# Kernel optimization log

Hardware: AMD Instinct MI355X
Metric: run time of the kernel (lower is better)

Reference implementation:

```python
import jax, jax.numpy as jnp
import numpy as np

B, N, D = 4, 2048, 1024
H, DH = 16, 64
MAX_POS_EMB = 256
TOPK = 64


def setup_inputs() -> dict:
    key = jax.random.key(0)
    ks = jax.random.split(key, 8)
    s = 0.02
    inner = H * DH
    return {
        "x": jax.random.normal(ks[0], (B, N, D), jnp.float32),
        "gating_mask": jax.random.uniform(ks[1], (B, 1, N, 1), jnp.float32),
        "Wq": jax.random.normal(ks[2], (D, inner), jnp.float32) * s,
        "bq": jnp.zeros((inner,), jnp.float32),
        "Wkv": jax.random.normal(ks[3], (D, 2 * inner), jnp.float32) * s,
        "bkv": jnp.zeros((2 * inner,), jnp.float32),
        "Wo": jax.random.normal(ks[4], (inner, D), jnp.float32) * s,
        "bo": jnp.zeros((D,), jnp.float32),
        "rel_emb": jax.random.normal(ks[5], (MAX_POS_EMB, DH), jnp.float32) * s,
        "mask": jnp.ones((B, N), bool),
        "sparse_topk": TOPK,
    }


def reference(x, gating_mask, Wq, bq, Wkv, bkv, Wo, bo, rel_emb, mask, sparse_topk):
    b, n, d = x.shape
    h, dh = H, DH
    scale = dh ** -0.5
    mask_val = -jnp.finfo(x.dtype).max

    # projections -> [b, h, n, dh]
    q = (x @ Wq + bq).reshape(b, n, h, dh).transpose(0, 2, 1, 3)
    kv = x @ Wkv + bkv
    k = kv[..., : h * dh].reshape(b, n, h, dh).transpose(0, 2, 1, 3)
    v = kv[..., h * dh:].reshape(b, n, h, dh).transpose(0, 2, 1, 3)

    dots = jnp.einsum("bhid,bhjd->bhij", q, k) * scale  # [b,h,n,n]

    # relative positional bias: q . E[clip(i-j+M, 0, M-1)]
    seq = jnp.arange(n)
    dist = jnp.clip(seq[:, None] - seq[None, :] + MAX_POS_EMB, 0, MAX_POS_EMB - 1)
    qE = jnp.einsum("bhid,rd->bhir", q, rel_emb) * scale  # [b,h,n,R]
    pos_attn = jnp.take_along_axis(qE, dist[None, None, :, :], axis=-1)  # [b,h,n,n]
    dots = dots + pos_attn

    # padding mask: mask_i * mask_j
    full_mask = mask[:, None, :, None] & mask[:, None, None, :]
    dots = jnp.where(full_mask, dots, mask_val)

    # topk sparsification: keep only scores >= k-th largest per row
    top = jax.lax.top_k(dots, sparse_topk)[0]  # [b,h,n,topk]
    vk = top[..., -1:]
    dots = jnp.where(dots < vk, mask_val, dots)

    attn = jax.nn.softmax(dots, axis=-1)
    attn = attn * gating_mask

    out = jnp.einsum("bhij,bhjd->bhid", attn, v)
    out = out.transpose(0, 2, 1, 3).reshape(b, n, h * dh)
    return out @ Wo + bo
```

## Files before the change

### kernel.cpp

```cpp
#include <hip/hip_runtime.h>
#include <stdint.h>


typedef __attribute__((ext_vector_type(8))) short short8;
typedef __attribute__((ext_vector_type(4))) float floatx4;

#define Bn   4
#define Nn   2048
#define Hn   16
#define BHn  (Bn*Hn)
#define DELTA 0.00125f

__device__ __forceinline__ float bf2f(unsigned short u) {
  union { unsigned int i; float f; } v; v.i = ((unsigned int)u) << 16; return v.f;
}
__device__ __forceinline__ unsigned short f2bf(float f) {
  union { float f; unsigned int i; } v; v.f = f;
  unsigned int r = v.i + 0x7fffu + ((v.i >> 16) & 1u);
  return (unsigned short)(r >> 16);
}
__device__ __forceinline__ floatx4 mfma16(short8 a, short8 b, floatx4 c) {
  return __builtin_amdgcn_mfma_f32_16x16x32_bf16(a, b, c, 0, 0, 0);
}
__device__ __forceinline__ void split2(float x, unsigned short& h, unsigned short& m) {
  h = f2bf(x);
  m = f2bf(x - bf2f(h));
}
__device__ __forceinline__ void split3(float x, unsigned short& h, unsigned short& m, unsigned short& l) {
  h = f2bf(x);
  float r = x - bf2f(h);
  m = f2bf(r);
  l = f2bf(r - bf2f(m));
}

__global__ __launch_bounds__(256)
void transpose_split3(const float* __restrict__ W,
                      unsigned short* __restrict__ T0,
                      unsigned short* __restrict__ T1,
                      unsigned short* __restrict__ T2,
                      int K, int Ncols)
{
  __shared__ float tile[32][33];
  int k0 = blockIdx.y * 32, n0 = blockIdx.x * 32;
  int tx = threadIdx.x & 31, ty = threadIdx.x >> 5;
  for (int s = 0; s < 32; s += 8)
    tile[ty + s][tx] = W[(size_t)(k0 + ty + s) * Ncols + n0 + tx];
  __syncthreads();
  for (int s = 0; s < 32; s += 8) {
    float x = tile[tx][ty + s];
    unsigned short h, m, l;
    split3(x, h, m, l);
    size_t o = (size_t)(n0 + ty + s) * K + k0 + tx;
    T0[o] = h; T1[o] = m; T2[o] = l;
  }
}

__global__ __launch_bounds__(256)
void transpose_split2(const float* __restrict__ W,
                      unsigned short* __restrict__ T0,
                      unsigned short* __restrict__ T1,
                      int K, int Ncols)
{
  __shared__ float tile[32][33];
  int k0 = blockIdx.y * 32, n0 = blockIdx.x * 32;
  int tx = threadIdx.x & 31, ty = threadIdx.x >> 5;
  for (int s = 0; s < 32; s += 8)
    tile[ty + s][tx] = W[(size_t)(k0 + ty + s) * Ncols + n0 + tx];
  __syncthreads();
  for (int s = 0; s < 32; s += 8) {
    float x = tile[tx][ty + s];
    unsigned short h, m;
    split2(x, h, m);
    size_t o = (size_t)(n0 + ty + s) * K + k0 + tx;
    T0[o] = h; T1[o] = m;
  }
}

__global__ __launch_bounds__(256)
void convert_bf16(const float* __restrict__ in, unsigned short* __restrict__ outp, int n) {
  int i = blockIdx.x * 256 + threadIdx.x;
  if (i < n) outp[i] = f2bf(in[i]);
}

__global__ __launch_bounds__(256)
void gemm_qkv(const float* __restrict__ A,
              const unsigned short* __restrict__ B0,
              const unsigned short* __restrict__ B1,
              const unsigned short* __restrict__ B2,
              const float* __restrict__ bias,
              float* __restrict__ O32,
              unsigned short* __restrict__ Oh,
              unsigned short* __restrict__ Om,
              unsigned short* __restrict__ Vh,
              int K, float scale)
{
  __shared__ unsigned short lA[3][128 * 40];
  __shared__ unsigned short lB[3][128 * 40];
  const int tid = threadIdx.x;
  const int lane = tid & 63;
  const int m0 = blockIdx.y * 128, n0 = blockIdx.x * 128;
  const int wid = tid >> 6, wm = wid >> 1, wn = wid & 1;
  const int fr = lane & 15, fq = lane >> 4;
  floatx4 acc[4][4] = {};

  for (int k0 = 0; k0 < K; k0 += 32) {
    __syncthreads();
    #pragma unroll
    for (int p = 0; p < 2; p++) {
      int c = tid + p * 256;
      int row = c >> 2, kc = (c & 3) * 8;
      size_t go = (size_t)(m0 + row) * K + k0 + kc;
      float4 v0 = *(const float4*)&A[go];
      float4 v1 = *(const float4*)&A[go + 4];
      union { unsigned short u[8]; uint4 q; } hh, mm, ll;
      float xs[8] = {v0.x, v0.y, v0.z, v0.w, v1.x, v1.y, v1.z, v1.w};
      #pragma unroll
      for (int e = 0; e < 8; e++) split3(xs[e], hh.u[e], mm.u[e], ll.u[e]);
      *(uint4*)&lA[0][row * 40 + kc] = hh.q;
      *(uint4*)&lA[1][row * 40 + kc] = mm.q;
      *(uint4*)&lA[2][row * 40 + kc] = ll.q;
      size_t bo = (size_t)(n0 + row) * K + k0 + kc;
      *(uint4*)&lB[0][row * 40 + kc] = *(const uint4*)&B0[bo];
      *(uint4*)&lB[1][row * 40 + kc] = *(const uint4*)&B1[bo];
      *(uint4*)&lB[2][row * 40 + kc] = *(const uint4*)&B2[bo];
    }
    __syncthreads();
    short8 af[3][4], bfr[3][4];
    #pragma unroll
    for (int s = 0; s < 3; s++)
      #pragma unroll
      for (int t = 0; t < 4; t++) {
        af[s][t]  = *(const short8*)&lA[s][(wm * 64 + t * 16 + fr) * 40 + 8 * fq];
        bfr[s][t] = *(const short8*)&lB[s][(wn * 64 + t * 16 + fr) * 40 + 8 * fq];
      }
    #pragma unroll
    for (int mi = 0; mi < 4; mi++)
      #pragma unroll
      for (int ni = 0; ni < 4; ni++) {
        acc[mi][ni] = mfma16(af[0][mi], bfr[0][ni], acc[mi][ni]);
        acc[mi][ni] = mfma16(af[0][mi], bfr[1][ni], acc[mi][ni]);
        acc[mi][ni] = mfma16(af[1][mi], bfr[0][ni], acc[mi][ni]);
        acc[mi][ni] = mfma16(af[1][mi], bfr[1][ni], acc[mi][ni]);
        acc[mi][ni] = mfma16(af[0][mi], bfr[2][ni], acc[mi][ni]);
        acc[mi][ni] = mfma16(af[2][mi], bfr[0][ni], acc[mi][ni]);
      }
  }
  #pragma unroll
  for (int mi = 0; mi < 4; mi++)
    #pragma unroll
    for (int ni = 0; ni < 4; ni++) {
      int nl = n0 + wn * 64 + ni * 16 + fr;
      float bv = bias[nl];
      #pragma unroll
      for (int rg = 0; rg < 4; rg++) {
        int ml = m0 + wm * 64 + mi * 16 + fq * 4 + rg;
        float val = (acc[mi][ni][rg] + bv) * scale;
        int bb = ml >> 11, ii = ml & 2047;
        int hh2 = (nl & 1023) >> 6, dd = nl & 63;
        size_t idx = (((size_t)bb * Hn + hh2) * Nn + ii) * 64 + dd;
        if (nl < 1024) {
          O32[idx] = val;
          unsigned short h, m;
          split2(val, h, m);
          Oh[idx] = h; Om[idx] = m;
        } else {
          Vh[idx] = f2bf(val);
        }
      }
    }
}

__global__ __launch_bounds__(256)
void gemm_out(const float* __restrict__ A,
              const unsigned short* __restrict__ B0,
              const unsigned short* __restrict__ B1,
              const float* __restrict__ bias,
              float* __restrict__ O32,
              int Ncols, int K)
{
  __shared__ unsigned short lA[2][128 * 40];
  __shared__ unsigned short lB[2][128 * 40];
  const int tid = threadIdx.x;
  const int lane = tid & 63;
  const int m0 = blockIdx.y * 128, n0 = blockIdx.x * 128;
  const int wid = tid >> 6, wm = wid >> 1, wn = wid & 1;
  const int fr = lane & 15, fq = lane >> 4;
  floatx4 acc[4][4] = {};

  for (int k0 = 0; k0 < K; k0 += 32) {
    __syncthreads();
    #pragma unroll
    for (int p = 0; p < 2; p++) {
      int c = tid + p * 256;
      int row = c >> 2, kc = (c & 3) * 8;
      size_t go = (size_t)(m0 + row) * K + k0 + kc;
      float4 v0 = *(const float4*)&A[go];
      float4 v1 = *(const float4*)&A[go + 4];
      union { unsigned short u[8]; uint4 q; } hh, mm;
      float xs[8] = {v0.x, v0.y, v0.z, v0.w, v1.x, v1.y, v1.z, v1.w};
      #pragma unroll
      for (int e = 0; e < 8; e++) split2(xs[e], hh.u[e], mm.u[e]);
      *(uint4*)&lA[0][row * 40 + kc] = hh.q;
      *(uint4*)&lA[1][row * 40 + kc] = mm.q;
      size_t bo = (size_t)(n0 + row) * K + k0 + kc;
      *(uint4*)&lB[0][row * 40 + kc] = *(const uint4*)&B0[bo];
      *(uint4*)&lB[1][row * 40 + kc] = *(const uint4*)&B1[bo];
    }
    __syncthreads();
    short8 af[2][4], bfr[2][4];
    #pragma unroll
    for (int s = 0; s < 2; s++)
      #pragma unroll
      for (int t = 0; t < 4; t++) {
        af[s][t]  = *(const short8*)&lA[s][(wm * 64 + t * 16 + fr) * 40 + 8 * fq];
        bfr[s][t] = *(const short8*)&lB[s][(wn * 64 + t * 16 + fr) * 40 + 8 * fq];
      }
    #pragma unroll
    for (int mi = 0; mi < 4; mi++)
      #pragma unroll
      for (int ni = 0; ni < 4; ni++) {
        acc[mi][ni] = mfma16(af[0][mi], bfr[0][ni], acc[mi][ni]);
        acc[mi][ni] = mfma16(af[0][mi], bfr[1][ni], acc[mi][ni]);
        acc[mi][ni] = mfma16(af[1][mi], bfr[0][ni], acc[mi][ni]);
      }
  }
  #pragma unroll
  for (int mi = 0; mi < 4; mi++)
    #pragma unroll
    for (int ni = 0; ni < 4; ni++) {
      int nl = n0 + wn * 64 + ni * 16 + fr;
      float bv = bias[nl];
      #pragma unroll
      for (int rg = 0; rg < 4; rg++) {
        int ml = m0 + wm * 64 + mi * 16 + fq * 4 + rg;
        O32[(size_t)ml * Ncols + nl] = acc[mi][ni][rg] + bv;
      }
    }
}

__global__ __launch_bounds__(512, 4)
void attn_k(const unsigned short* __restrict__ qh,
            const unsigned short* __restrict__ qm,
            const unsigned short* __restrict__ kh,
            const unsigned short* __restrict__ km,
            const unsigned short* __restrict__ vh,
            const float* __restrict__ q32,
            const float* __restrict__ k32,
            const unsigned short* __restrict__ relbf,
            const float* __restrict__ rel32,
            const float* __restrict__ gating,
            const int* __restrict__ topkp,
            float* __restrict__ inner)
{
  extern __shared__ char smem[];
  _Float16* S = (_Float16*)smem;
  unsigned short* KtH = (unsigned short*)(smem + 65536);
  unsigned short* KtM = KtH + 4096;
  _Float16* qE = (_Float16*)KtH;

  const int ib = blockIdx.x, bh = blockIdx.y;
  const int i0 = ib * 16;
  const int b = bh >> 4, h = bh & 15;
  const int tid = threadIdx.x;
  const int lane = tid & 63, w = tid >> 6;
  const int fr = lane & 15, fq = lane >> 4;
  const int topk = topkp[0];

  const size_t qoff = ((size_t)bh * Nn + i0) * 64;
  const size_t qf = qoff + (size_t)fr * 64 + 8 * fq;
  const short8 aqh0 = *(const short8*)&qh[qf];
  const short8 aqh1 = *(const short8*)&qh[qf + 32];
  const short8 aqm0 = *(const short8*)&qm[qf];
  const short8 aqm1 = *(const short8*)&qm[qf + 32];

  for (int jt = 0; jt < 32; jt++) {
    __syncthreads();
    {
      int row = tid >> 3, dc = (tid & 7) * 8;
      size_t g = ((size_t)bh * Nn + jt * 64 + row) * 64 + dc;
      *(uint4*)&KtH[row * 64 + dc] = *(const uint4*)&kh[g];
      *(uint4*)&KtM[row * 64 + dc] = *(const uint4*)&km[g];
    }
    __syncthreads();
    if ((jt & 1) == (w >> 2)) {
      int wc = w & 3;
      int kb = (wc * 16 + fr) * 64 + 8 * fq;
      short8 kh0 = *(const short8*)&KtH[kb];
      short8 kh1 = *(const short8*)&KtH[kb + 32];
      short8 km0 = *(const short8*)&KtM[kb];
      short8 km1 = *(const short8*)&KtM[kb + 32];
      floatx4 c = {};
      c = mfma16(aqh0, kh0, c); c = mfma16(aqh1, kh1, c);
      c = mfma16(aqh0, km0, c); c = mfma16(aqh1, km1, c);
      c = mfma16(aqm0, kh0, c); c = mfma16(aqm1, kh1, c);
      #pragma unroll
      for (int rg = 0; rg < 4; rg++)
        S[(fq * 4 + rg) * 2048 + jt * 64 + wc * 16 + fr] = (_Float16)c[rg];
    }
  }
  __syncthreads();

  #pragma unroll
  for (int rs = 0; rs < 2; rs++) {
    int r0 = (w * 2 + rs) * 16;
    size_t rf = (size_t)(r0 + fr) * 64 + 8 * fq;
    short8 rb0 = *(const short8*)&relbf[rf];
    short8 rb1 = *(const short8*)&relbf[rf + 32];
    floatx4 c = {};
    c = mfma16(aqh0, rb0, c); c = mfma16(aqh1, rb1, c);
    c = mfma16(aqm0, rb0, c); c = mfma16(aqm1, rb1, c);
    #pragma unroll
    for (int rg = 0; rg < 4; rg++)
      qE[(fq * 4 + rg) * 256 + r0 + fr] = (_Float16)c[rg];
  }
  __syncthreads();

  #pragma unroll 1
  for (int rr = 0; rr < 2; rr++) {
    const int r = w * 2 + rr;
    const int i = i0 + r;
    const _Float16* Srow = S + r * 2048;
    const _Float16* qErow = qE + r * 256;

    float key[32];
    float mx = -3.0e38f, sum = 0.f, ssq = 0.f;
    #pragma unroll
    for (int e = 0; e < 16; e++) {
      int j0 = 2 * lane + 128 * e;
      union { unsigned int u; _Float16 hx[2]; } sv;
      sv.u = *(const unsigned int*)&Srow[j0];
      int r0i = i - j0 + 256;
      int c0 = r0i < 0 ? 0 : (r0i > 255 ? 255 : r0i);
      int r1i = r0i - 1;
      int c1 = r1i < 0 ? 0 : (r1i > 255 ? 255 : r1i);
      float s0 = (float)sv.hx[0] + (float)qErow[c0];
      float s1 = (float)sv.hx[1] + (float)qErow[c1];
      key[2 * e] = s0; key[2 * e + 1] = s1;
      mx = fmaxf(mx, fmaxf(s0, s1));
      sum += s0 + s1;
      ssq += s0 * s0 + s1 * s1;
    }
    #pragma unroll
    for (int d = 1; d < 64; d <<= 1) {
      mx = fmaxf(mx, __shfl_xor(mx, d));
      sum += __shfl_xor(sum, d);
      ssq += __shfl_xor(ssq, d);
    }
    const float mu = sum * (1.f / 2048.f);
    const float sg = sqrtf(fmaxf(ssq * (1.f / 2048.f) - mu * mu, 0.f)) + 1e-9f;

    auto cntGE = [&](float u) -> int {
      int c = 0;
      #pragma unroll
      for (int e = 0; e < 32; e++) c += (key[e] >= u) ? 1 : 0;
      #pragma unroll
      for (int d = 1; d < 64; d <<= 1) c += __shfl_xor(c, d);
      return c;
    };

    float lo = mu + 1.6f * sg;
    float hi = mx + fabsf(mx) * 1e-6f + 1e-20f;
    int cl = cntGE(lo);
    #pragma unroll 1
    for (int t = 0; t < 6 && cl < topk; t++) {
      hi = lo; lo -= (0.8f + 0.4f * t) * sg; cl = cntGE(lo);
    }
    if (cl < topk) lo = -3.0e38f;
    #pragma unroll 1
    for (int it = 0; it < 10; it++) {
      float mid = 0.5f * (lo + hi);
      if (cntGE(mid) >= topk) lo = mid; else hi = mid;
    }
    const float C = hi + 2.0f * DELTA;
    const float L = lo - 2.0f * DELTA;

    char* sb = (char*)Srow;
    float* Pl = (float*)(sb);
    int*   Jl = (int*)(sb + 512);
    float* Sx = (float*)(sb + 1024);
    int*   Jc = (int*)(sb + 1280);
    asm volatile("" ::: "memory");
    const unsigned long long lmlt = (1ull << lane) - 1ull;

    int base = 0;
    #pragma unroll
    for (int e2 = 0; e2 < 32; e2++) {
      bool dk = key[e2] >= C;
      unsigned long long mk = __ballot(dk);
      if (dk) {
        int pos = base + __popcll(mk & lmlt);
        Pl[pos] = key[e2]; Jl[pos] = 2 * lane + 128 * (e2 >> 1) + (e2 & 1);
      }
      base += __popcll(mk);
    }
    int mcand = 0;
    #pragma unroll
    for (int e2 = 0; e2 < 32; e2++) {
      bool cd = (key[e2] >= L) && (key[e2] < C);
      unsigned long long mk = __ballot(cd);
      if (cd) {
        int pos = mcand + __popcll(mk & lmlt);
        if (pos < 64) Jc[pos] = 2 * lane + 128 * (e2 >> 1) + (e2 & 1);
      }
      mcand += __popcll(mk);
    }
    if (mcand > 64) mcand = 64;
    asm volatile("" ::: "memory");

    const size_t qrow = ((size_t)bh * Nn + i) * 64 + lane;
    const double qv = (double)q32[qrow];
    #pragma unroll 1
    for (int c2 = 0; c2 < mcand; c2++) {
      int j = Jc[c2];
      int ridx = i - j + 256;
      ridx = ridx < 0 ? 0 : (ridx > 255 ? 255 : ridx);
      size_t krow = ((size_t)bh * Nn + j) * 64 + lane;
      double t = qv * ((double)k32[krow] + (double)rel32[ridx * 64 + lane]);
      #pragma unroll
      for (int d = 1; d < 64; d <<= 1) t += __shfl_xor(t, d);
      if (lane == 0) Sx[c2] = (float)t;
    }
    asm volatile("" ::: "memory");

    const int need = topk - base;
    float myx = (lane < mcand) ? Sx[lane] : -3.0e38f;
    int rank = 0;
    #pragma unroll 1
    for (int c2 = 0; c2 < mcand; c2++) {
      float o = Sx[c2];
      rank += (o > myx || (o == myx && c2 < lane)) ? 1 : 0;
    }
    bool ck = (lane < mcand) && (rank < need);
    unsigned long long mk2 = __ballot(ck);
    if (ck) {
      int pos = base + __popcll(mk2 & lmlt);
      Pl[pos] = myx; Jl[pos] = Jc[lane];
    }
    base += __popcll(mk2);
    const int nk = base;
    asm volatile("" ::: "memory");

    float p = 0.f;
    if (lane < nk) { p = __expf(Pl[lane] - mx); Pl[lane] = p; }
    float psum = p;
    #pragma unroll
    for (int d = 1; d < 64; d <<= 1) psum += __shfl_xor(psum, d);
    const float coef = gating[(size_t)b * Nn + i] / psum;
    asm volatile("" ::: "memory");

    float a0 = 0, a1 = 0, a2 = 0, a3 = 0;
    const size_t vb = (size_t)bh * Nn * 64;
    int t4 = nk & ~3;
    #pragma unroll 1
    for (int t = 0; t < t4; t += 4) {
      float p0 = Pl[t], p1 = Pl[t + 1], p2 = Pl[t + 2], p3 = Pl[t + 3];
      int j0 = Jl[t], j1 = Jl[t + 1], j2 = Jl[t + 2], j3 = Jl[t + 3];
      a0 += p0 * bf2f(vh[vb + (size_t)j0 * 64 + lane]);
      a1 += p1 * bf2f(vh[vb + (size_t)j1 * 64 + lane]);
      a2 += p2 * bf2f(vh[vb + (size_t)j2 * 64 + lane]);
      a3 += p3 * bf2f(vh[vb + (size_t)j3 * 64 + lane]);
    }
    for (int t = t4; t < nk; t++)
      a0 += Pl[t] * bf2f(vh[vb + (size_t)Jl[t] * 64 + lane]);
    float outv = (a0 + a1 + a2 + a3) * coef;
    inner[((size_t)b * Nn + i) * 1024 + h * 64 + lane] = outv;
  }
}

extern "C" void kernel_launch(void* const* d_in, const int* in_sizes, int n_in,
                              void* d_out, int out_size, void* d_ws, size_t ws_size,
                              hipStream_t stream) {
  const float* x      = (const float*)d_in[0];
  const float* gating = (const float*)d_in[1];
  const float* Wq     = (const float*)d_in[2];
  const float* bq     = (const float*)d_in[3];
  const float* Wkv    = (const float*)d_in[4];
  const float* bkv    = (const float*)d_in[5];
  const float* Wo     = (const float*)d_in[6];
  const float* bo     = (const float*)d_in[7];
  const float* rel    = (const float*)d_in[8];
  const int*   topk   = (const int*)d_in[10];
  float* out = (float*)d_out;

  char* ws = (char*)d_ws;
  size_t off = 0;
  auto alloc = [&](size_t bytes) -> void* {
    void* p = ws + off; off += (bytes + 255) & ~(size_t)255; return p;
  };
  unsigned short* Wqt0 = (unsigned short*)alloc(1024ull * 1024 * 2);
  unsigned short* Wqt1 = (unsigned short*)alloc(1024ull * 1024 * 2);
  unsigned short* Wqt2 = (unsigned short*)alloc(1024ull * 1024 * 2);
  unsigned short* Wkt0 = (unsigned short*)alloc(2048ull * 1024 * 2);
  unsigned short* Wkt1 = (unsigned short*)alloc(2048ull * 1024 * 2);
  unsigned short* Wkt2 = (unsigned short*)alloc(2048ull * 1024 * 2);
  unsigned short* Wot0 = (unsigned short*)alloc(1024ull * 1024 * 2);
  unsigned short* Wot1 = (unsigned short*)alloc(1024ull * 1024 * 2);
  unsigned short* relbf = (unsigned short*)alloc(256ull * 64 * 2);
  float* q32 = (float*)alloc((size_t)BHn * Nn * 64 * 4);
  float* k32 = (float*)alloc((size_t)BHn * Nn * 64 * 4);
  unsigned short* qhb = (unsigned short*)alloc((size_t)BHn * Nn * 64 * 2);
  unsigned short* qmb = (unsigned short*)alloc((size_t)BHn * Nn * 64 * 2);
  unsigned short* khb = (unsigned short*)alloc((size_t)BHn * Nn * 64 * 2);
  unsigned short* kmb = (unsigned short*)alloc((size_t)BHn * Nn * 64 * 2);
  unsigned short* vhb = (unsigned short*)alloc((size_t)BHn * Nn * 64 * 2);
  float* inner = (float*)alloc((size_t)Bn * Nn * 1024 * 4);
  if (off > ws_size) return;

  size_t shmem = 65536 + 16384;
  (void)hipFuncSetAttribute((const void*)attn_k,
                            hipFuncAttributeMaxDynamicSharedMemorySize, (int)shmem);

  transpose_split3<<<dim3(32, 32), 256, 0, stream>>>(Wq, Wqt0, Wqt1, Wqt2, 1024, 1024);
  transpose_split3<<<dim3(64, 32), 256, 0, stream>>>(Wkv, Wkt0, Wkt1, Wkt2, 1024, 2048);
  transpose_split2<<<dim3(32, 32), 256, 0, stream>>>(Wo, Wot0, Wot1, 1024, 1024);
  convert_bf16<<<dim3(64), 256, 0, stream>>>(rel, relbf, 256 * 64);

  gemm_qkv<<<dim3(8, 64), 256, 0, stream>>>(x, Wqt0, Wqt1, Wqt2, bq,
      q32, qhb, qmb, qhb, 1024, 0.125f);
  gemm_qkv<<<dim3(16, 64), 256, 0, stream>>>(x, Wkt0, Wkt1, Wkt2, bkv,
      k32, khb, kmb, vhb, 1024, 1.0f);

  attn_k<<<dim3(128, 64), 512, shmem, stream>>>(qhb, qmb, khb, kmb, vhb,
      q32, k32, relbf, rel, gating, topk, inner);

  gemm_out<<<dim3(8, 64), 256, 0, stream>>>(inner, Wot0, Wot1, bo,
      out, 1024, 1024);
}
```

Measured before the change: 1.294 ms.

## Cut V-projection precision, swizzle LDS, and process two attention rows per warp

The QKV GEMM skips the third split term and the hi*mid MFMA for V-column blocks and stores V as fp16 instead of bf16. The attention kernel XOR-swizzles the K tile, the score matrix and the qE layout in LDS to avoid bank conflicts. It also handles two query rows per wavefront at once, with packed dual counting in the threshold bisection, and uses a precomputed fast path for clipped relative-position indices. Tie handling at the k-th value is changed to keep every element equal to the threshold. The trade-off is lower V precision and higher register pressure from the doubled per-row state.

```diff
diff --git a/kernel.cpp b/kernel.cpp
--- a/kernel.cpp
+++ b/kernel.cpp
@@ -91,7 +91,7 @@
               float* __restrict__ O32,
               unsigned short* __restrict__ Oh,
               unsigned short* __restrict__ Om,
-              unsigned short* __restrict__ Vh,
+              _Float16* __restrict__ Vh,
               int K, float scale)
 {
   __shared__ unsigned short lA[3][128 * 40];
@@ -99,6 +99,7 @@
   const int tid = threadIdx.x;
   const int lane = tid & 63;
   const int m0 = blockIdx.y * 128, n0 = blockIdx.x * 128;
+  const bool vblk = (n0 >= 1024);
   const int wid = tid >> 6, wm = wid >> 1, wn = wid & 1;
   const int fr = lane & 15, fq = lane >> 4;
   floatx4 acc[4][4] = {};
@@ -118,31 +119,41 @@
       for (int e = 0; e < 8; e++) split3(xs[e], hh.u[e], mm.u[e], ll.u[e]);
       *(uint4*)&lA[0][row * 40 + kc] = hh.q;
       *(uint4*)&lA[1][row * 40 + kc] = mm.q;
-      *(uint4*)&lA[2][row * 40 + kc] = ll.q;
       size_t bo = (size_t)(n0 + row) * K + k0 + kc;
       *(uint4*)&lB[0][row * 40 + kc] = *(const uint4*)&B0[bo];
       *(uint4*)&lB[1][row * 40 + kc] = *(const uint4*)&B1[bo];
-      *(uint4*)&lB[2][row * 40 + kc] = *(const uint4*)&B2[bo];
+      if (!vblk) {
+        *(uint4*)&lA[2][row * 40 + kc] = ll.q;
+        *(uint4*)&lB[2][row * 40 + kc] = *(const uint4*)&B2[bo];
+      }
     }
     __syncthreads();
-    short8 af[3][4], bfr[3][4];
-    #pragma unroll
-    for (int s = 0; s < 3; s++)
-      #pragma unroll
-      for (int t = 0; t < 4; t++) {
-        af[s][t]  = *(const short8*)&lA[s][(wm * 64 + t * 16 + fr) * 40 + 8 * fq];
-        bfr[s][t] = *(const short8*)&lB[s][(wn * 64 + t * 16 + fr) * 40 + 8 * fq];
+    short8 af0[4], af1[4], af2[4], bf0[4], bf1[4], bf2v[4];
+    #pragma unroll
+    for (int t = 0; t < 4; t++) {
+      int ao = (wm * 64 + t * 16 + fr) * 40 + 8 * fq;
+      int bo2 = (wn * 64 + t * 16 + fr) * 40 + 8 * fq;
+      af0[t] = *(const short8*)&lA[0][ao];
+      af1[t] = *(const short8*)&lA[1][ao];
+      bf0[t] = *(const short8*)&lB[0][bo2];
+      bf1[t] = *(const short8*)&lB[1][bo2];
+      if (!vblk) {
+        af2[t] = *(const short8*)&lA[2][ao];
+        bf2v[t] = *(const short8*)&lB[2][bo2];
       }
+    }
     #pragma unroll
     for (int mi = 0; mi < 4; mi++)
       #pragma unroll
       for (int ni = 0; ni < 4; ni++) {
-        acc[mi][ni] = mfma16(af[0][mi], bfr[0][ni], acc[mi][ni]);
-        acc[mi][ni] = mfma16(af[0][mi], bfr[1][ni], acc[mi][ni]);
-        acc[mi][ni] = mfma16(af[1][mi], bfr[0][ni], acc[mi][ni]);
-        acc[mi][ni] = mfma16(af[1][mi], bfr[1][ni], acc[mi][ni]);
-        acc[mi][ni] = mfma16(af[0][mi], bfr[2][ni], acc[mi][ni]);
-        acc[mi][ni] = mfma16(af[2][mi], bfr[0][ni], acc[mi][ni]);
+        acc[mi][ni] = mfma16(af0[mi], bf0[ni], acc[mi][ni]);
+        acc[mi][ni] = mfma16(af0[mi], bf1[ni], acc[mi][ni]);
+        acc[mi][ni] = mfma16(af1[mi], bf0[ni], acc[mi][ni]);
+        if (!vblk) {
+          acc[mi][ni] = mfma16(af1[mi], bf1[ni], acc[mi][ni]);
+          acc[mi][ni] = mfma16(af0[mi], bf2v[ni], acc[mi][ni]);
+          acc[mi][ni] = mfma16(af2[mi], bf0[ni], acc[mi][ni]);
+        }
       }
   }
   #pragma unroll
@@ -158,13 +169,13 @@
         int bb = ml >> 11, ii = ml & 2047;
         int hh2 = (nl & 1023) >> 6, dd = nl & 63;
         size_t idx = (((size_t)bb * Hn + hh2) * Nn + ii) * 64 + dd;
-        if (nl < 1024) {
+        if (!vblk) {
           O32[idx] = val;
           unsigned short h, m;
           split2(val, h, m);
           Oh[idx] = h; Om[idx] = m;
         } else {
-          Vh[idx] = f2bf(val);
+          Vh[idx] = (_Float16)val;
         }
       }
     }
@@ -243,7 +254,7 @@
             const unsigned short* __restrict__ qm,
             const unsigned short* __restrict__ kh,
             const unsigned short* __restrict__ km,
-            const unsigned short* __restrict__ vh,
+            const _Float16* __restrict__ vh,
             const float* __restrict__ q32,
             const float* __restrict__ k32,
             const unsigned short* __restrict__ relbf,
@@ -276,195 +287,259 @@
   for (int jt = 0; jt < 32; jt++) {
     __syncthreads();
     {
-      int row = tid >> 3, dc = (tid & 7) * 8;
-      size_t g = ((size_t)bh * Nn + jt * 64 + row) * 64 + dc;
-      *(uint4*)&KtH[row * 64 + dc] = *(const uint4*)&kh[g];
-      *(uint4*)&KtM[row * 64 + dc] = *(const uint4*)&km[g];
+      int row = tid >> 3, ch = tid & 7;
+      int dst = row * 64 + ((ch ^ (row & 7)) * 8);
+      size_t g = ((size_t)bh * Nn + jt * 64 + row) * 64 + ch * 8;
+      *(uint4*)&KtH[dst] = *(const uint4*)&kh[g];
+      *(uint4*)&KtM[dst] = *(const uint4*)&km[g];
     }
     __syncthreads();
     if ((jt & 1) == (w >> 2)) {
       int wc = w & 3;
-      int kb = (wc * 16 + fr) * 64 + 8 * fq;
-      short8 kh0 = *(const short8*)&KtH[kb];
-      short8 kh1 = *(const short8*)&KtH[kb + 32];
-      short8 km0 = *(const short8*)&KtM[kb];
-      short8 km1 = *(const short8*)&KtM[kb + 32];
+      int row16 = wc * 16 + fr, r7 = fr & 7;
+      int b0 = row16 * 64 + ((fq ^ r7) * 8);
+      int b1 = row16 * 64 + (((fq + 4) ^ r7) * 8);
+      short8 kh0 = *(const short8*)&KtH[b0];
+      short8 kh1 = *(const short8*)&KtH[b1];
+      short8 km0 = *(const short8*)&KtM[b0];
+      short8 km1 = *(const short8*)&KtM[b1];
       floatx4 c = {};
       c = mfma16(aqh0, kh0, c); c = mfma16(aqh1, kh1, c);
       c = mfma16(aqh0, km0, c); c = mfma16(aqh1, km1, c);
       c = mfma16(aqm0, kh0, c); c = mfma16(aqm1, kh1, c);
+      int colsw = jt * 64 + ((wc ^ fq) * 16) + fr;
       #pragma unroll
       for (int rg = 0; rg < 4; rg++)
-        S[(fq * 4 + rg) * 2048 + jt * 64 + wc * 16 + fr] = (_Float16)c[rg];
+        S[(fq * 4 + rg) * 2048 + colsw] = (_Float16)c[rg];
     }
   }
   __syncthreads();
 
   #pragma unroll
   for (int rs = 0; rs < 2; rs++) {
-    int r0 = (w * 2 + rs) * 16;
-    size_t rf = (size_t)(r0 + fr) * 64 + 8 * fq;
+    int rq = w * 2 + rs;
+    size_t rf = (size_t)(rq * 16 + fr) * 64 + 8 * fq;
     short8 rb0 = *(const short8*)&relbf[rf];
     short8 rb1 = *(const short8*)&relbf[rf + 32];
     floatx4 c = {};
     c = mfma16(aqh0, rb0, c); c = mfma16(aqh1, rb1, c);
     c = mfma16(aqm0, rb0, c); c = mfma16(aqm1, rb1, c);
+    int colsw = ((rq ^ fq) * 16) + fr;
     #pragma unroll
     for (int rg = 0; rg < 4; rg++)
-      qE[(fq * 4 + rg) * 256 + r0 + fr] = (_Float16)c[rg];
+      qE[(fq * 4 + rg) * 256 + colsw] = (_Float16)c[rg];
   }
   __syncthreads();
 
-  #pragma unroll 1
-  for (int rr = 0; rr < 2; rr++) {
-    const int r = w * 2 + rr;
-    const int i = i0 + r;
-    const _Float16* Srow = S + r * 2048;
-    const _Float16* qErow = qE + r * 256;
-
-    float key[32];
-    float mx = -3.0e38f, sum = 0.f, ssq = 0.f;
-    #pragma unroll
-    for (int e = 0; e < 16; e++) {
-      int j0 = 2 * lane + 128 * e;
-      union { unsigned int u; _Float16 hx[2]; } sv;
-      sv.u = *(const unsigned int*)&Srow[j0];
-      int r0i = i - j0 + 256;
-      int c0 = r0i < 0 ? 0 : (r0i > 255 ? 255 : r0i);
-      int r1i = r0i - 1;
-      int c1 = r1i < 0 ? 0 : (r1i > 255 ? 255 : r1i);
-      float s0 = (float)sv.hx[0] + (float)qErow[c0];
-      float s1 = (float)sv.hx[1] + (float)qErow[c1];
-      key[2 * e] = s0; key[2 * e + 1] = s1;
-      mx = fmaxf(mx, fmaxf(s0, s1));
-      sum += s0 + s1;
-      ssq += s0 * s0 + s1 * s1;
+  const int r0 = w * 2, r1 = r0 + 1;
+  const int ii0 = i0 + r0, ii1 = i0 + r1;
+  const int X = (w >> 1) << 4;
+  _Float16* S0 = S + r0 * 2048;
+  _Float16* S1 = S + r1 * 2048;
+  const _Float16* qE0 = qE + r0 * 256;
+  const _Float16* qE1 = qE + r1 * 256;
+  const float cA0 = (float)qE0[255 ^ X], cC0 = (float)qE0[X];
+  const float cA1 = (float)qE1[255 ^ X], cC1 = (float)qE1[X];
+  const int swl = (2 * lane) ^ X;
+
+  float k0v[32], k1v[32];
+  float mx0 = -3.0e38f, mx1 = -3.0e38f;
+  float sm0 = 0.f, sm1 = 0.f, sq0 = 0.f, sq1 = 0.f;
+  #pragma unroll
+  for (int e = 0; e < 16; e++) {
+    const int jb = 128 * e;
+    union { unsigned int u; _Float16 hx[2]; } u0, u1;
+    u0.u = *(const unsigned int*)&S0[jb + swl];
+    u1.u = *(const unsigned int*)&S1[jb + swl];
+    const int j0 = jb + 2 * lane;
+    float e00, e01, e10, e11;
+    if (jb + 127 <= ii0) { e00 = cA0; e01 = cA0; }
+    else if (jb >= ii0 + 256) { e00 = cC0; e01 = cC0; }
+    else {
+      int c0 = ii0 - j0 + 256; c0 = c0 < 0 ? 0 : (c0 > 255 ? 255 : c0);
+      int c1 = ii0 - j0 + 255; c1 = c1 < 0 ? 0 : (c1 > 255 ? 255 : c1);
+      e00 = (float)qE0[c0 ^ X]; e01 = (float)qE0[c1 ^ X];
+    }
+    if (jb + 127 <= ii1) { e10 = cA1; e11 = cA1; }
+    else if (jb >= ii1 + 256) { e10 = cC1; e11 = cC1; }
+    else {
+      int c0 = ii1 - j0 + 256; c0 = c0 < 0 ? 0 : (c0 > 255 ? 255 : c0);
+      int c1 = ii1 - j0 + 255; c1 = c1 < 0 ? 0 : (c1 > 255 ? 255 : c1);
+      e10 = (float)qE1[c0 ^ X]; e11 = (float)qE1[c1 ^ X];
+    }
+    float a0 = (float)u0.hx[0] + e00, a1 = (float)u0.hx[1] + e01;
+    float b0 = (float)u1.hx[0] + e10, b1 = (float)u1.hx[1] + e11;
+    k0v[2 * e] = a0; k0v[2 * e + 1] = a1;
+    k1v[2 * e] = b0; k1v[2 * e + 1] = b1;
+    mx0 = fmaxf(mx0, fmaxf(a0, a1)); mx1 = fmaxf(mx1, fmaxf(b0, b1));
+    sm0 += a0 + a1; sm1 += b0 + b1;
+    sq0 = fmaf(a0, a0, fmaf(a1, a1, sq0));
+    sq1 = fmaf(b0, b0, fmaf(b1, b1, sq1));
+  }
+  #pragma unroll
+  for (int d = 1; d < 64; d <<= 1) {
+    mx0 = fmaxf(mx0, __shfl_xor(mx0, d));
+    mx1 = fmaxf(mx1, __shfl_xor(mx1, d));
+    sm0 += __shfl_xor(sm0, d);
+    sm1 += __shfl_xor(sm1, d);
+    sq0 += __shfl_xor(sq0, d);
+    sq1 += __shfl_xor(sq1, d);
+  }
+  const float mu0 = sm0 * (1.f / 2048.f), mu1 = sm1 * (1.f / 2048.f);
+  const float sg0 = sqrtf(fmaxf(sq0 * (1.f / 2048.f) - mu0 * mu0, 0.f)) + 1e-9f;
+  const float sg1 = sqrtf(fmaxf(sq1 * (1.f / 2048.f) - mu1 * mu1, 0.f)) + 1e-9f;
+
+  auto cnt2 = [&](float t0, float t1, int& o0, int& o1) {
+    int cc = 0;
+    #pragma unroll
+    for (int t = 0; t < 32; t++)
+      cc += (k0v[t] >= t0 ? 1 : 0) + (k1v[t] >= t1 ? 0x10000 : 0);
+    #pragma unroll
+    for (int d = 1; d < 64; d <<= 1) cc += __shfl_xor(cc, d);
+    o0 = cc & 0xffff; o1 = cc >> 16;
+  };
+
+  float lo0 = mu0 + sg0, lo1 = mu1 + sg1;
+  float hi0 = mx0 + fabsf(mx0) * 1e-6f + 1e-20f;
+  float hi1 = mx1 + fabsf(mx1) * 1e-6f + 1e-20f;
+  int c0n, c1n;
+  cnt2(lo0, lo1, c0n, c1n);
+  if ((c0n < topk) || (c1n < topk)) {
+    if (c0n < topk) lo0 = mu0;
+    if (c1n < topk) lo1 = mu1;
+    int c0b, c1b;
+    cnt2(lo0, lo1, c0b, c1b);
+    if (c0b < topk) lo0 = mu0 - 20.f * sg0;
+    if (c1b < topk) lo1 = mu1 - 20.f * sg1;
+  }
+  #pragma unroll 1
+  for (int it = 0; it < 10; it++) {
+    float m0 = 0.5f * (lo0 + hi0), m1 = 0.5f * (lo1 + hi1);
+    cnt2(m0, m1, c0n, c1n);
+    if (c0n >= topk) lo0 = m0; else hi0 = m0;
+    if (c1n >= topk) lo1 = m1; else hi1 = m1;
+  }
+  const float C0 = hi0 + 2.f * DELTA, L0 = lo0 - 2.f * DELTA;
+  const float C1 = hi1 + 2.f * DELTA, L1 = lo1 - 2.f * DELTA;
+
+  char* sb0 = (char*)S0;
+  char* sb1 = (char*)S1;
+  float* Pl0 = (float*)sb0;          int* Jl0 = (int*)(sb0 + 512);
+  float* Sx0 = (float*)(sb0 + 1024); int* Jc0 = (int*)(sb0 + 1280);
+  float* Pl1 = (float*)sb1;          int* Jl1 = (int*)(sb1 + 512);
+  float* Sx1 = (float*)(sb1 + 1024); int* Jc1 = (int*)(sb1 + 1280);
+  asm volatile("" ::: "memory");
+  const unsigned long long lmlt = (1ull << lane) - 1ull;
+
+  int base0 = 0, base1 = 0, mc0 = 0, mc1 = 0;
+  #pragma unroll
+  for (int t = 0; t < 32; t++) {
+    const int j = 2 * lane + 128 * (t >> 1) + (t & 1);
+    bool dk0 = k0v[t] >= C0;
+    bool cd0 = (k0v[t] >= L0) && !dk0;
+    unsigned long long mk = __ballot(dk0);
+    if (dk0) { int pos = base0 + __popcll(mk & lmlt); Pl0[pos] = k0v[t]; Jl0[pos] = j; }
+    base0 += __popcll(mk);
+    mk = __ballot(cd0);
+    if (cd0) { int pos = mc0 + __popcll(mk & lmlt); if (pos < 64) Jc0[pos] = j; }
+    mc0 += __popcll(mk);
+    bool dk1 = k1v[t] >= C1;
+    bool cd1 = (k1v[t] >= L1) && !dk1;
+    mk = __ballot(dk1);
+    if (dk1) { int pos = base1 + __popcll(mk & lmlt); Pl1[pos] = k1v[t]; Jl1[pos] = j; }
+    base1 += __popcll(mk);
+    mk = __ballot(cd1);
+    if (cd1) { int pos = mc1 + __popcll(mk & lmlt); if (pos < 64) Jc1[pos] = j; }
+    mc1 += __popcll(mk);
+  }
+  if (mc0 > 64) mc0 = 64;
+  if (mc1 > 64) mc1 = 64;
+  asm volatile("" ::: "memory");
+
+  const double qv0 = (double)q32[((size_t)bh * Nn + ii0) * 64 + lane];
+  const double qv1 = (double)q32[((size_t)bh * Nn + ii1) * 64 + lane];
+  const int mcx = mc0 > mc1 ? mc0 : mc1;
+  #pragma unroll 1
+  for (int c2 = 0; c2 < mcx; c2++) {
+    double t0 = 0.0, t1 = 0.0;
+    if (c2 < mc0) {
+      int j = Jc0[c2];
+      int ridx = ii0 - j + 256; ridx = ridx < 0 ? 0 : (ridx > 255 ? 255 : ridx);
+      t0 = qv0 * ((double)k32[((size_t)bh * Nn + j) * 64 + lane] +
+                  (double)rel32[ridx * 64 + lane]);
+    }
+    if (c2 < mc1) {
+      int j = Jc1[c2];
+      int ridx = ii1 - j + 256; ridx = ridx < 0 ? 0 : (ridx > 255 ? 255 : ridx);
+      t1 = qv1 * ((double)k32[((size_t)bh * Nn + j) * 64 + lane] +
+                  (double)rel32[ridx * 64 + lane]);
     }
     #pragma unroll
     for (int d = 1; d < 64; d <<= 1) {
-      mx = fmaxf(mx, __shfl_xor(mx, d));
-      sum += __shfl_xor(sum, d);
-      ssq += __shfl_xor(ssq, d);
-    }
-    const float mu = sum * (1.f / 2048.f);
-    const float sg = sqrtf(fmaxf(ssq * (1.f / 2048.f) - mu * mu, 0.f)) + 1e-9f;
-
-    auto cntGE = [&](float u) -> int {
-      int c = 0;
-      #pragma unroll
-      for (int e = 0; e < 32; e++) c += (key[e] >= u) ? 1 : 0;
-      #pragma unroll
-      for (int d = 1; d < 64; d <<= 1) c += __shfl_xor(c, d);
-      return c;
-    };
-
-    float lo = mu + 1.6f * sg;
-    float hi = mx + fabsf(mx) * 1e-6f + 1e-20f;
-    int cl = cntGE(lo);
-    #pragma unroll 1
-    for (int t = 0; t < 6 && cl < topk; t++) {
-      hi = lo; lo -= (0.8f + 0.4f * t) * sg; cl = cntGE(lo);
-    }
-    if (cl < topk) lo = -3.0e38f;
-    #pragma unroll 1
-    for (int it = 0; it < 10; it++) {
-      float mid = 0.5f * (lo + hi);
-      if (cntGE(mid) >= topk) lo = mid; else hi = mid;
-    }
-    const float C = hi + 2.0f * DELTA;
-    const float L = lo - 2.0f * DELTA;
-
-    char* sb = (char*)Srow;
-    float* Pl = (float*)(sb);
-    int*   Jl = (int*)(sb + 512);
-    float* Sx = (float*)(sb + 1024);
-    int*   Jc = (int*)(sb + 1280);
-    asm volatile("" ::: "memory");
-    const unsigned long long lmlt = (1ull << lane) - 1ull;
-
-    int base = 0;
-    #pragma unroll
-    for (int e2 = 0; e2 < 32; e2++) {
-      bool dk = key[e2] >= C;
-      unsigned long long mk = __ballot(dk);
-      if (dk) {
-        int pos = base + __popcll(mk & lmlt);
-        Pl[pos] = key[e2]; Jl[pos] = 2 * lane + 128 * (e2 >> 1) + (e2 & 1);
-      }
-      base += __popcll(mk);
-    }
-    int mcand = 0;
-    #pragma unroll
-    for (int e2 = 0; e2 < 32; e2++) {
-      bool cd = (key[e2] >= L) && (key[e2] < C);
-      unsigned long long mk = __ballot(cd);
-      if (cd) {
-        int pos = mcand + __popcll(mk & lmlt);
-        if (pos < 64) Jc[pos] = 2 * lane + 128 * (e2 >> 1) + (e2 & 1);
-      }
-      mcand += __popcll(mk);
-    }
-    if (mcand > 64) mcand = 64;
-    asm volatile("" ::: "memory");
-
-    const size_t qrow = ((size_t)bh * Nn + i) * 64 + lane;
-    const double qv = (double)q32[qrow];
-    #pragma unroll 1
-    for (int c2 = 0; c2 < mcand; c2++) {
-      int j = Jc[c2];
-      int ridx = i - j + 256;
-      ridx = ridx < 0 ? 0 : (ridx > 255 ? 255 : ridx);
-      size_t krow = ((size_t)bh * Nn + j) * 64 + lane;
-      double t = qv * ((double)k32[krow] + (double)rel32[ridx * 64 + lane]);
-      #pragma unroll
-      for (int d = 1; d < 64; d <<= 1) t += __shfl_xor(t, d);
-      if (lane == 0) Sx[c2] = (float)t;
-    }
-    asm volatile("" ::: "memory");
-
-    const int need = topk - base;
-    float myx = (lane < mcand) ? Sx[lane] : -3.0e38f;
-    int rank = 0;
-    #pragma unroll 1
-    for (int c2 = 0; c2 < mcand; c2++) {
-      float o = Sx[c2];
-      rank += (o > myx || (o == myx && c2 < lane)) ? 1 : 0;
-    }
-    bool ck = (lane < mcand) && (rank < need);
-    unsigned long long mk2 = __ballot(ck);
-    if (ck) {
-      int pos = base + __popcll(mk2 & lmlt);
-      Pl[pos] = myx; Jl[pos] = Jc[lane];
-    }
-    base += __popcll(mk2);
-    const int nk = base;
-    asm volatile("" ::: "memory");
-
-    float p = 0.f;
-    if (lane < nk) { p = __expf(Pl[lane] - mx); Pl[lane] = p; }
-    float psum = p;
-    #pragma unroll
-    for (int d = 1; d < 64; d <<= 1) psum += __shfl_xor(psum, d);
-    const float coef = gating[(size_t)b * Nn + i] / psum;
-    asm volatile("" ::: "memory");
-
-    float a0 = 0, a1 = 0, a2 = 0, a3 = 0;
-    const size_t vb = (size_t)bh * Nn * 64;
-    int t4 = nk & ~3;
-    #pragma unroll 1
-    for (int t = 0; t < t4; t += 4) {
-      float p0 = Pl[t], p1 = Pl[t + 1], p2 = Pl[t + 2], p3 = Pl[t + 3];
-      int j0 = Jl[t], j1 = Jl[t + 1], j2 = Jl[t + 2], j3 = Jl[t + 3];
-      a0 += p0 * bf2f(vh[vb + (size_t)j0 * 64 + lane]);
-      a1 += p1 * bf2f(vh[vb + (size_t)j1 * 64 + lane]);
-      a2 += p2 * bf2f(vh[vb + (size_t)j2 * 64 + lane]);
-      a3 += p3 * bf2f(vh[vb + (size_t)j3 * 64 + lane]);
-    }
-    for (int t = t4; t < nk; t++)
-      a0 += Pl[t] * bf2f(vh[vb + (size_t)Jl[t] * 64 + lane]);
-    float outv = (a0 + a1 + a2 + a3) * coef;
-    inner[((size_t)b * Nn + i) * 1024 + h * 64 + lane] = outv;
-  }
+      t0 += __shfl_xor(t0, d);
+      t1 += __shfl_xor(t1, d);
+    }
+    if (lane == 0) {
+      if (c2 < mc0) Sx0[c2] = (float)t0;
+      if (c2 < mc1) Sx1[c2] = (float)t1;
+    }
+  }
+  asm volatile("" ::: "memory");
+
+  const int need0 = topk - base0, need1 = topk - base1;
+  float myx0 = (lane < mc0) ? Sx0[lane] : -3.0e38f;
+  float myx1 = (lane < mc1) ? Sx1[lane] : -3.0e38f;
+  int rank0 = 0, rank1 = 0;
+  #pragma unroll 1
+  for (int c2 = 0; c2 < mcx; c2++) {
+    if (c2 < mc0) { float o = Sx0[c2]; rank0 += (o > myx0 || (o == myx0 && c2 < lane)) ? 1 : 0; }
+    if (c2 < mc1) { float o = Sx1[c2]; rank1 += (o > myx1 || (o == myx1 && c2 < lane)) ? 1 : 0; }
+  }
+  unsigned long long bm0 = __ballot((lane < mc0) && (rank0 == need0 - 1));
+  unsigned long long bm1 = __ballot((lane < mc1) && (rank1 == need1 - 1));
+  float vk0 = bm0 ? __shfl(myx0, (int)__ffsll(bm0) - 1) : 3.0e38f;
+  float vk1 = bm1 ? __shfl(myx1, (int)__ffsll(bm1) - 1) : 3.0e38f;
+  bool ck0 = (lane < mc0) && ((rank0 < need0) || (myx0 == vk0));
+  bool ck1 = (lane < mc1) && ((rank1 < need1) || (myx1 == vk1));
+  unsigned long long km0 = __ballot(ck0), km1 = __ballot(ck1);
+  if (ck0) { int pos = base0 + __popcll(km0 & lmlt); Pl0[pos] = myx0; Jl0[pos] = Jc0[lane]; }
+  if (ck1) { int pos = base1 + __popcll(km1 & lmlt); Pl1[pos] = myx1; Jl1[pos] = Jc1[lane]; }
+  const int nk0 = base0 + __popcll(km0);
+  const int nk1 = base1 + __popcll(km1);
+  asm volatile("" ::: "memory");
+
+  float ps0 = 0.f, ps1 = 0.f;
+  #pragma unroll 1
+  for (int t = lane; t < nk0; t += 64) { float p = __expf(Pl0[t] - mx0); Pl0[t] = p; ps0 += p; }
+  #pragma unroll 1
+  for (int t = lane; t < nk1; t += 64) { float p = __expf(Pl1[t] - mx1); Pl1[t] = p; ps1 += p; }
+  #pragma unroll
+  for (int d = 1; d < 64; d <<= 1) {
+    ps0 += __shfl_xor(ps0, d);
+    ps1 += __shfl_xor(ps1, d);
+  }
+  const float coef0 = gating[(size_t)b * Nn + ii0] / ps0;
+  const float coef1 = gating[(size_t)b * Nn + ii1] / ps1;
+  asm volatile("" ::: "memory");
+
+  const _Float16* vbp = vh + (size_t)bh * Nn * 64 + lane;
+  float a00 = 0.f, a01 = 0.f, a10 = 0.f, a11 = 0.f;
+  const int nmin = (nk0 < nk1 ? nk0 : nk1) & ~1;
+  #pragma unroll 1
+  for (int t = 0; t < nmin; t += 2) {
+    float p00 = Pl0[t], p01 = Pl0[t + 1]; int j00 = Jl0[t], j01 = Jl0[t + 1];
+    float p10 = Pl1[t], p11 = Pl1[t + 1]; int j10 = Jl1[t], j11 = Jl1[t + 1];
+    a00 += p00 * (float)vbp[(size_t)j00 * 64];
+    a01 += p01 * (float)vbp[(size_t)j01 * 64];
+    a10 += p10 * (float)vbp[(size_t)j10 * 64];
+    a11 += p11 * (float)vbp[(size_t)j11 * 64];
+  }
+  #pragma unroll 1
+  for (int t = nmin; t < nk0; t++) a00 += Pl0[t] * (float)vbp[(size_t)Jl0[t] * 64];
+  #pragma unroll 1
+  for (int t = nmin; t < nk1; t++) a10 += Pl1[t] * (float)vbp[(size_t)Jl1[t] * 64];
+  inner[((size_t)b * Nn + ii0) * 1024 + h * 64 + lane] = (a00 + a01) * coef0;
+  inner[((size_t)b * Nn + ii1) * 1024 + h * 64 + lane] = (a10 + a11) * coef1;
 }
 
 extern "C" void kernel_launch(void* const* d_in, const int* in_sizes, int n_in,
@@ -502,7 +577,7 @@
   unsigned short* qmb = (unsigned short*)alloc((size_t)BHn * Nn * 64 * 2);
   unsigned short* khb = (unsigned short*)alloc((size_t)BHn * Nn * 64 * 2);
   unsigned short* kmb = (unsigned short*)alloc((size_t)BHn * Nn * 64 * 2);
-  unsigned short* vhb = (unsigned short*)alloc((size_t)BHn * Nn * 64 * 2);
+  _Float16* vhb = (_Float16*)alloc((size_t)BHn * Nn * 64 * 2);
   float* inner = (float*)alloc((size_t)Bn * Nn * 1024 * 4);
   if (off > ws_size) return;
 
@@ -516,7 +591,7 @@
   convert_bf16<<<dim3(64), 256, 0, stream>>>(rel, relbf, 256 * 64);
 
   gemm_qkv<<<dim3(8, 64), 256, 0, stream>>>(x, Wqt0, Wqt1, Wqt2, bq,
-      q32, qhb, qmb, qhb, 1024, 0.125f);
+      q32, qhb, qmb, vhb, 1024, 0.125f);
   gemm_qkv<<<dim3(16, 64), 256, 0, stream>>>(x, Wkt0, Wkt1, Wkt2, bkv,
       k32, khb, kmb, vhb, 1024, 1.0f);
 
```

After: 1.298 ms. Within noise of the previous version (+0.3%).
